# Optimization experiments

Hardware: AMD Instinct MI355X
Metric: run time of the kernel (lower is better)

Reference implementation:

```python
import jax, jax.numpy as jnp
import numpy as np

E = 512        # embed_dim
H = 8          # num_heads
DH = E // H    # head dim
CONCAT = 2 * E # 1024
HID = CONCAT // 2  # 512
OUT = 256      # out_dim
B = 65536


def setup_inputs() -> dict:
    key = jax.random.key(0)
    ks = jax.random.split(key, 12)
    s = lambda fan_in: 1.0 / np.sqrt(fan_in)
    return {
        "visual_emb": jax.random.normal(ks[0], (B, E), jnp.float32),
        "text_emb": jax.random.normal(ks[1], (B, E), jnp.float32),
        # nn.MultiheadAttention params (torch layout: Linear weight is (out,in))
        "in_proj_w": jax.random.uniform(ks[2], (3 * E, E), jnp.float32, -s(E), s(E)),
        "in_proj_b": jnp.zeros((3 * E,), jnp.float32),
        "out_proj_w": jax.random.uniform(ks[3], (E, E), jnp.float32, -s(E), s(E)),
        "out_proj_b": jnp.zeros((E,), jnp.float32),
        # MLP
        "mlp_w1": jax.random.uniform(ks[4], (HID, CONCAT), jnp.float32, -s(CONCAT), s(CONCAT)),
        "mlp_b1": jax.random.uniform(ks[5], (HID,), jnp.float32, -s(CONCAT), s(CONCAT)),
        "mlp_w2": jax.random.uniform(ks[6], (OUT, HID), jnp.float32, -s(HID), s(HID)),
        "mlp_b2": jax.random.uniform(ks[7], (OUT,), jnp.float32, -s(HID), s(HID)),
        # LayerNorm
        "ln_gamma": jnp.ones((OUT,), jnp.float32),
        "ln_beta": jnp.zeros((OUT,), jnp.float32),
    }


def reference(visual_emb, text_emb, in_proj_w, in_proj_b, out_proj_w, out_proj_b,
              mlp_w1, mlp_b1, mlp_w2, mlp_b2, ln_gamma, ln_beta):
    # (B, 2, E) stack of modalities
    x = jnp.stack([visual_emb, text_emb], axis=1)
    # fused QKV projection
    qkv = jnp.einsum("bse,fe->bsf", x, in_proj_w) + in_proj_b  # (B,2,3E)
    q, k, v = jnp.split(qkv, 3, axis=-1)
    # split heads -> (B,H,2,DH)
    split = lambda t: t.reshape(t.shape[0], 2, H, DH).transpose(0, 2, 1, 3)
    q, k, v = split(q), split(k), split(v)
    scores = jnp.einsum("bhqd,bhkd->bhqk", q, k) / jnp.sqrt(jnp.float32(DH))
    attn = jax.nn.softmax(scores, axis=-1)          # (B,H,2,2)
    ctx = jnp.einsum("bhqk,bhkd->bhqd", attn, v)    # (B,H,2,DH)
    ctx = ctx.transpose(0, 2, 1, 3).reshape(-1, 2, E)
    attended = jnp.einsum("bse,fe->bsf", ctx, out_proj_w) + out_proj_b
    weights = attn.mean(axis=1)                     # average over heads (torch default)
    flat = attended.reshape(attended.shape[0], CONCAT)
    h = jax.nn.gelu(flat @ mlp_w1.T + mlp_b1, approximate=False)
    o = h @ mlp_w2.T + mlp_b2                       # (B, OUT)
    mu = o.mean(axis=-1, keepdims=True)
    var = o.var(axis=-1, keepdims=True)
    fused = (o - mu) * jax.lax.rsqrt(var + 1e-5) * ln_gamma + ln_beta
    return fused, weights
```

## Files before the change

### kernel.cpp

```cpp
#include <hip/hip_runtime.h>
#include <hip/hip_bf16.h>
#include <math.h>

#define BATCH   65536L
#define EDIM    512
#define QKVDIM  1536
#define CONCATD 1024
#define HIDD    512
#define OUTD    256

typedef __bf16 bf16_t;
typedef __bf16 bf16x8 __attribute__((ext_vector_type(8)));
typedef __bf16 bf16x4 __attribute__((ext_vector_type(4)));
typedef float  floatx4 __attribute__((ext_vector_type(4)));

static_assert(sizeof(bf16x8) == 16, "bf16x8 must be 16B");

__device__ __forceinline__ void gload16(const void* g, void* l) {
  __builtin_amdgcn_global_load_lds(
      (__attribute__((address_space(1))) void*)(g),
      (__attribute__((address_space(3))) void*)(l), 16, 0, 0);
}

__global__ __launch_bounds__(256) void convert_x_kernel(
    const float* __restrict__ vis, const float* __restrict__ txt,
    bf16_t* __restrict__ dst) {
  long idx = (long)blockIdx.x * 256 + threadIdx.x;
  long t = idx >> 6;
  int  c = (int)(idx & 63) * 8;
  long b = t >> 1;
  const float* src = ((t & 1) ? txt : vis) + b * EDIM + c;
  float4 f0 = *(const float4*)src;
  float4 f1 = *(const float4*)(src + 4);
  bf16x8 o;
  o[0] = (bf16_t)f0.x; o[1] = (bf16_t)f0.y; o[2] = (bf16_t)f0.z; o[3] = (bf16_t)f0.w;
  o[4] = (bf16_t)f1.x; o[5] = (bf16_t)f1.y; o[6] = (bf16_t)f1.z; o[7] = (bf16_t)f1.w;
  *(bf16x8*)(dst + t * EDIM + c) = o;
}

__global__ __launch_bounds__(256) void convert_w_kernel(
    const float* __restrict__ wq, const float* __restrict__ w2,
    bf16_t* __restrict__ dst) {
  long idx = ((long)blockIdx.x * 256 + threadIdx.x) * 8;
  const long n0 = 786432;
  const float* src; long off;
  if (idx < n0) { src = wq; off = idx; }
  else          { src = w2; off = idx - n0; }
  float4 f0 = *(const float4*)(src + off);
  float4 f1 = *(const float4*)(src + off + 4);
  bf16x8 o;
  o[0] = (bf16_t)f0.x; o[1] = (bf16_t)f0.y; o[2] = (bf16_t)f0.z; o[3] = (bf16_t)f0.w;
  o[4] = (bf16_t)f1.x; o[5] = (bf16_t)f1.y; o[6] = (bf16_t)f1.z; o[7] = (bf16_t)f1.w;
  *(bf16x8*)(dst + idx) = o;
}

__global__ __launch_bounds__(256) void wc_kernel(
    const float* __restrict__ w1, const float* __restrict__ wo,
    bf16_t* __restrict__ wc) {
  int n = blockIdx.x;
  int t = threadIdx.x;
  const float* w1v = w1 + (long)n * 1024;
  const float* w1t = w1v + 512;
  float a0 = 0.f, a1 = 0.f, a2 = 0.f, a3 = 0.f;
  for (int f = 0; f < 512; f++) {
    float wv = w1v[f], wt = w1t[f];
    float x0 = wo[f * 512 + t], x1 = wo[f * 512 + t + 256];
    a0 += wv * x0; a1 += wv * x1;
    a2 += wt * x0; a3 += wt * x1;
  }
  bf16_t* out = wc + (long)n * 1024;
  out[t]        = (bf16_t)a0;
  out[t + 256]  = (bf16_t)a1;
  out[t + 512]  = (bf16_t)a2;
  out[t + 768]  = (bf16_t)a3;
}

__global__ __launch_bounds__(256) void bc_kernel(
    const float* __restrict__ w1, const float* __restrict__ bo,
    const float* __restrict__ b1, float* __restrict__ bc) {
  int n = blockIdx.x * 256 + threadIdx.x;
  const float* w1row = w1 + (long)n * 1024;
  float acc = b1[n];
  for (int f = 0; f < 512; f++)
    acc += (w1row[f] + w1row[512 + f]) * bo[f];
  bc[n] = acc;
}

template<int EPI>
__global__ __launch_bounds__(512, 2) void gemm256_kernel(
    const bf16_t* __restrict__ A, const bf16_t* __restrict__ Bt,
    const float* __restrict__ bias, bf16_t* __restrict__ C,
    int M, int N, int K, int ntiles) {
  __shared__ __attribute__((aligned(16))) bf16_t lds[4 * 16384];
  int bid = blockIdx.x;
  {
    const int nwg = gridDim.x;
    if ((nwg & 7) == 0) bid = (bid & 7) * (nwg >> 3) + (bid >> 3);
  }
  const int mt   = bid / ntiles;
  const int nt   = bid % ntiles;
  const int tid  = threadIdx.x;
  const int wave = tid >> 6;
  const int lane = tid & 63;
  const int WM   = wave >> 2;
  const int WN   = wave & 3;

  floatx4 acc[8][4];
  #pragma unroll
  for (int i = 0; i < 8; i++)
    #pragma unroll
    for (int j = 0; j < 4; j++) acc[i][j] = (floatx4){0.f, 0.f, 0.f, 0.f};

  const int srow = wave * 16 + (lane >> 2);
  const int scol = (((lane & 3) ^ ((lane >> 3) & 3)) * 8);
  const bf16_t* Ag0 = A  + (long)(mt * 256 + srow) * K + scol;
  const bf16_t* Ag1 = Ag0 + 128L * K;
  const bf16_t* Bg0 = Bt + (long)(nt * 256 + srow) * K + scol;
  const bf16_t* Bg1 = Bg0 + 128L * K;
  const int woff = wave * 512;

  const int m_l = lane & 15;
  const int kq  = (((lane >> 4) ^ ((m_l >> 1) & 3)) * 8);
  const int Kt  = K >> 5;
  const int Km  = Kt - 1;

#define STAGE(tk, slot) do {                                    \
    const long ko_ = (long)(tk) * 32;                           \
    bf16_t* s_ = lds + (slot) * 16384;                          \
    gload16(Ag0 + ko_, s_ + woff);                              \
    gload16(Ag1 + ko_, s_ + 4096 + woff);                       \
    gload16(Bg0 + ko_, s_ + 8192 + woff);                       \
    gload16(Bg1 + ko_, s_ + 12288 + woff);                      \
  } while (0)

  STAGE(0, 0);
  STAGE(1, 1);
  STAGE(2, 2);

  for (int t = 0; t < Kt; t++) {
    STAGE((t + 3) & Km, (t + 3) & 3);
    asm volatile("s_waitcnt vmcnt(12)" ::: "memory");
    __builtin_amdgcn_s_barrier();
    asm volatile("" ::: "memory");

    const bf16_t* sl = lds + (t & 3) * 16384;
    bf16x8 a[8], b[4];
    #pragma unroll
    for (int i = 0; i < 8; i++)
      a[i] = *(const bf16x8*)&sl[(WM * 128 + i * 16 + m_l) * 32 + kq];
    #pragma unroll
    for (int j = 0; j < 4; j++)
      b[j] = *(const bf16x8*)&sl[8192 + (WN * 64 + j * 16 + m_l) * 32 + kq];
    #pragma unroll
    for (int i = 0; i < 8; i++)
      #pragma unroll
      for (int j = 0; j < 4; j++)
        acc[i][j] = __builtin_amdgcn_mfma_f32_16x16x32_bf16(a[i], b[j], acc[i][j], 0, 0, 0);

    asm volatile("" ::: "memory");
    __builtin_amdgcn_s_barrier();
    asm volatile("" ::: "memory");
  }
#undef STAGE

  const int col_l = lane & 15;
  const int row_q = (lane >> 4) * 4;
  float bj[4];
  #pragma unroll
  for (int j = 0; j < 4; j++)
    bj[j] = bias[nt * 256 + WN * 64 + j * 16 + col_l];
  #pragma unroll
  for (int i = 0; i < 8; i++) {
    #pragma unroll
    for (int r = 0; r < 4; r++) {
      long row = (long)(mt * 256 + WM * 128 + i * 16 + row_q + r);
      bf16_t* crow = C + row * N + nt * 256 + WN * 64 + col_l;
      #pragma unroll
      for (int j = 0; j < 4; j++) {
        float v = acc[i][j][r] + bj[j];
        if (EPI == 1) v = 0.5f * v * (1.0f + erff(v * 0.70710678118654752f));
        crow[j * 16] = (bf16_t)v;
      }
    }
  }
}

__global__ __launch_bounds__(256) void mlp2_ln_kernel(
    const bf16_t* __restrict__ A,
    const bf16_t* __restrict__ Bt,
    const float* __restrict__ bias,
    const float* __restrict__ gamma, const float* __restrict__ beta,
    float* __restrict__ out) {
  __shared__ __attribute__((aligned(16))) char smem[67072];
  bf16_t* sA   = (bf16_t*)smem;
  bf16_t* sB   = (bf16_t*)(smem + 4096);
  float*  Ot   = (float*)smem;
  float*  mu_s = (float*)(smem + 66560);
  float*  rs_s = (float*)(smem + 66816);

  const int tid  = threadIdx.x;
  const int wave = tid >> 6;
  const int lane = tid & 63;

  floatx4 acc[4][4];
  #pragma unroll
  for (int i = 0; i < 4; i++)
    #pragma unroll
    for (int j = 0; j < 4; j++) acc[i][j] = (floatx4){0.f, 0.f, 0.f, 0.f};

  const int srow = wave * 16 + (lane >> 2);
  const int scol = (((lane & 3) ^ ((lane >> 3) & 3)) * 8);
  const bf16_t* Ag = A  + ((long)blockIdx.x * 64 + srow) * 512 + scol;
  const bf16_t* Bg = Bt + (long)srow * 512 + scol;
  bf16_t* sAw = sA + wave * 16 * 32;

  const int m_l = lane & 15;
  const int kq  = (((lane >> 4) ^ ((m_l >> 1) & 3)) * 8);

  for (int k0 = 0; k0 < 512; k0 += 32) {
    __syncthreads();
    gload16(Ag + k0, sAw);
    gload16(Bg + k0,              sB + (0   + wave * 16) * 32);
    gload16(Bg + 64L * 512 + k0,  sB + (64  + wave * 16) * 32);
    gload16(Bg + 128L * 512 + k0, sB + (128 + wave * 16) * 32);
    gload16(Bg + 192L * 512 + k0, sB + (192 + wave * 16) * 32);
    __syncthreads();

    bf16x8 a[4], b[4];
    #pragma unroll
    for (int i = 0; i < 4; i++)
      a[i] = *(const bf16x8*)&sA[(i * 16 + m_l) * 32 + kq];
    #pragma unroll
    for (int j = 0; j < 4; j++)
      b[j] = *(const bf16x8*)&sB[(wave * 64 + j * 16 + m_l) * 32 + kq];
    #pragma unroll
    for (int i = 0; i < 4; i++)
      #pragma unroll
      for (int j = 0; j < 4; j++)
        acc[i][j] = __builtin_amdgcn_mfma_f32_16x16x32_bf16(a[i], b[j], acc[i][j], 0, 0, 0);
  }

  const int col_l = lane & 15;
  const int row_q = (lane >> 4) * 4;
  float bj[4];
  #pragma unroll
  for (int j = 0; j < 4; j++)
    bj[j] = bias[wave * 64 + j * 16 + col_l];
  __syncthreads();
  #pragma unroll
  for (int i = 0; i < 4; i++)
    #pragma unroll
    for (int r = 0; r < 4; r++)
      #pragma unroll
      for (int j = 0; j < 4; j++)
        Ot[(i * 16 + row_q + r) * 260 + wave * 64 + j * 16 + col_l] =
            acc[i][j][r] + bj[j];
  __syncthreads();

  {
    int row = tid >> 2, q = tid & 3;
    const float* p = Ot + row * 260 + q * 64;
    float s = 0.f, s2 = 0.f;
    #pragma unroll
    for (int c = 0; c < 64; c += 4) {
      float4 v = *(const float4*)(p + c);
      s  += v.x + v.y + v.z + v.w;
      s2 += v.x * v.x + v.y * v.y + v.z * v.z + v.w * v.w;
    }
    s  += __shfl_xor(s, 1);  s  += __shfl_xor(s, 2);
    s2 += __shfl_xor(s2, 1); s2 += __shfl_xor(s2, 2);
    if (q == 0) {
      float mu  = s * (1.0f / 256.0f);
      float var = s2 * (1.0f / 256.0f) - mu * mu;
      mu_s[row] = mu;
      rs_s[row] = rsqrtf(var + 1e-5f);
    }
  }
  __syncthreads();

  float4 g  = *(const float4*)(gamma + lane * 4);
  float4 be = *(const float4*)(beta + lane * 4);
  #pragma unroll
  for (int rr = 0; rr < 16; rr++) {
    int row = rr * 4 + wave;
    float mu = mu_s[row], rs = rs_s[row];
    float4 v = *(const float4*)(Ot + row * 260 + lane * 4);
    float4 res;
    res.x = (v.x - mu) * rs * g.x + be.x;
    res.y = (v.y - mu) * rs * g.y + be.y;
    res.z = (v.z - mu) * rs * g.z + be.z;
    res.w = (v.w - mu) * rs * g.w + be.w;
    *(float4*)(out + ((long)blockIdx.x * 64 + row) * 256 + lane * 4) = res;
  }
}

__global__ __launch_bounds__(256) void attn_kernel(
    const bf16_t* __restrict__ qkv, bf16_t* __restrict__ ctx,
    float* __restrict__ wout) {
  const int  lane = threadIdx.x & 63;
  const long b    = (long)blockIdx.x * 4 + (threadIdx.x >> 6);
  const bf16_t* base = qkv + b * 2 * QKVDIM;
  const int off = lane * 8;

  bf16x8 q0 = *(const bf16x8*)(base + off);
  bf16x8 k0 = *(const bf16x8*)(base + EDIM + off);
  bf16x8 v0 = *(const bf16x8*)(base + 2 * EDIM + off);
  bf16x8 q1 = *(const bf16x8*)(base + QKVDIM + off);
  bf16x8 k1 = *(const bf16x8*)(base + QKVDIM + EDIM + off);
  bf16x8 v1 = *(const bf16x8*)(base + QKVDIM + 2 * EDIM + off);

  float s00 = 0.f, s01 = 0.f, s10 = 0.f, s11 = 0.f;
  #pragma unroll
  for (int r = 0; r < 8; r++) {
    float x0 = (float)q0[r], x1 = (float)q1[r];
    float y0 = (float)k0[r], y1 = (float)k1[r];
    s00 += x0 * y0; s01 += x0 * y1; s10 += x1 * y0; s11 += x1 * y1;
  }
  #pragma unroll
  for (int m = 1; m < 8; m <<= 1) {
    s00 += __shfl_xor(s00, m); s01 += __shfl_xor(s01, m);
    s10 += __shfl_xor(s10, m); s11 += __shfl_xor(s11, m);
  }
  const float sc = 0.125f;
  s00 *= sc; s01 *= sc; s10 *= sc; s11 *= sc;
  float m0 = fmaxf(s00, s01), m1 = fmaxf(s10, s11);
  float e00 = __expf(s00 - m0), e01 = __expf(s01 - m0);
  float e10 = __expf(s10 - m1), e11 = __expf(s11 - m1);
  float d0 = e00 + e01, d1 = e10 + e11;
  float a00 = e00 / d0, a01 = e01 / d0, a10 = e10 / d1, a11 = e11 / d1;

  float r00 = a00, r01 = a01, r10 = a10, r11 = a11;
  #pragma unroll
  for (int m = 8; m < 64; m <<= 1) {
    r00 += __shfl_xor(r00, m); r01 += __shfl_xor(r01, m);
    r10 += __shfl_xor(r10, m); r11 += __shfl_xor(r11, m);
  }
  if (lane == 0) {
    float4 wv = make_float4(r00 * 0.125f, r01 * 0.125f, r10 * 0.125f, r11 * 0.125f);
    *(float4*)(wout + b * 4) = wv;
  }

  bf16x8 t0, t1;
  #pragma unroll
  for (int r = 0; r < 8; r++) {
    float f0 = (float)v0[r], f1 = (float)v1[r];
    t0[r] = (bf16_t)(a00 * f0 + a01 * f1);
    t1[r] = (bf16_t)(a10 * f0 + a11 * f1);
  }
  *(bf16x8*)(ctx + (b * 2) * EDIM + off)     = t0;
  *(bf16x8*)(ctx + (b * 2 + 1) * EDIM + off) = t1;
}

extern "C" void kernel_launch(void* const* d_in, const int* in_sizes, int n_in,
                              void* d_out, int out_size, void* d_ws, size_t ws_size,
                              hipStream_t stream) {
  (void)in_sizes; (void)n_in; (void)out_size;
  const float* vis   = (const float*)d_in[0];
  const float* txt   = (const float*)d_in[1];
  const float* w_qkv = (const float*)d_in[2];
  const float* b_qkv = (const float*)d_in[3];
  const float* w_out = (const float*)d_in[4];
  const float* b_out = (const float*)d_in[5];
  const float* w1    = (const float*)d_in[6];
  const float* b1    = (const float*)d_in[7];
  const float* w2    = (const float*)d_in[8];
  const float* b2    = (const float*)d_in[9];
  const float* gamma = (const float*)d_in[10];
  const float* beta  = (const float*)d_in[11];
  float* out_fused   = (float*)d_out;
  float* out_weights = out_fused + BATCH * OUTD;

  char* ws = (char*)d_ws;
  const size_t MB = 1024 * 1024;

  long Bc = BATCH;
  int  nch = 1;
  while (((size_t)(4 * MB) + (size_t)(8192UL * (unsigned long)Bc) > ws_size
          || Bc > 32768) && nch < 64) {
    Bc >>= 1; nch <<= 1;
  }

  bf16_t* wq_b = (bf16_t*)ws;
  bf16_t* w2_b = wq_b + 786432;
  bf16_t* wc_b = wq_b + 917504;
  float*  bc   = (float*)(ws + 3 * MB);
  convert_w_kernel<<<448, 256, 0, stream>>>(w_qkv, w2, wq_b);
  wc_kernel<<<512, 256, 0, stream>>>(w1, w_out, wc_b);
  bc_kernel<<<2, 256, 0, stream>>>(w1, b_out, b1, bc);

  bf16_t* reg1 = (bf16_t*)(ws + 4 * MB);
  bf16_t* reg2 = (bf16_t*)(ws + 4 * MB + (size_t)2048 * Bc);

  const long Tc = 2 * Bc;
  for (int c = 0; c < nch; c++) {
    const float* visc = vis + (long)c * Bc * EDIM;
    const float* txtc = txt + (long)c * Bc * EDIM;
    bf16_t* X   = reg1;
    bf16_t* QKV = reg2;
    bf16_t* CTX = reg1;
    bf16_t* H   = reg2;

    convert_x_kernel<<<(int)(Tc / 4), 256, 0, stream>>>(visc, txtc, X);
    gemm256_kernel<0><<<(int)(Tc / 256) * 6, 512, 0, stream>>>(
        X, wq_b, b_qkv, QKV, (int)Tc, QKVDIM, EDIM, 6);
    attn_kernel<<<(int)(Bc / 4), 256, 0, stream>>>(
        QKV, CTX, out_weights + (long)c * Bc * 4);
    gemm256_kernel<1><<<(int)(Bc / 256) * 2, 512, 0, stream>>>(
        CTX, wc_b, bc, H, (int)Bc, HIDD, CONCATD, 2);
    mlp2_ln_kernel<<<(int)(Bc / 64), 256, 0, stream>>>(
        H, w2_b, b2, gamma, beta, out_fused + (long)c * Bc * OUTD);
  }
}
```

Before: 872.1 us.

## Shrink GEMM tiles to 128x128 with 4 waves and triple-buffered LDS

Replaces the 256x256, 8-wave GEMM with a 128x128, 4-wave version. LDS use drops from a 4-stage to a 3-stage ring with a prefetch distance of 2, and s_setprio is raised around the MFMA block. Smaller tiles and less LDS per block are meant to raise occupancy and spread work more evenly across CUs. In exchange, arithmetic intensity per tile falls, so more global/L2 traffic is spent re-reading A and B.

```diff
diff --git a/kernel.cpp b/kernel.cpp
--- a/kernel.cpp
+++ b/kernel.cpp
@@ -87,11 +87,11 @@
 }
 
 template<int EPI>
-__global__ __launch_bounds__(512, 2) void gemm256_kernel(
+__global__ __launch_bounds__(256, 3) void gemm128_kernel(
     const bf16_t* __restrict__ A, const bf16_t* __restrict__ Bt,
     const float* __restrict__ bias, bf16_t* __restrict__ C,
     int M, int N, int K, int ntiles) {
-  __shared__ __attribute__((aligned(16))) bf16_t lds[4 * 16384];
+  __shared__ __attribute__((aligned(16))) bf16_t lds[3 * 8192];
   int bid = blockIdx.x;
   {
     const int nwg = gridDim.x;
@@ -102,21 +102,21 @@
   const int tid  = threadIdx.x;
   const int wave = tid >> 6;
   const int lane = tid & 63;
-  const int WM   = wave >> 2;
-  const int WN   = wave & 3;
-
-  floatx4 acc[8][4];
-  #pragma unroll
-  for (int i = 0; i < 8; i++)
+  const int wm   = wave >> 1;
+  const int wn   = wave & 1;
+
+  floatx4 acc[4][4];
+  #pragma unroll
+  for (int i = 0; i < 4; i++)
     #pragma unroll
     for (int j = 0; j < 4; j++) acc[i][j] = (floatx4){0.f, 0.f, 0.f, 0.f};
 
   const int srow = wave * 16 + (lane >> 2);
   const int scol = (((lane & 3) ^ ((lane >> 3) & 3)) * 8);
-  const bf16_t* Ag0 = A  + (long)(mt * 256 + srow) * K + scol;
-  const bf16_t* Ag1 = Ag0 + 128L * K;
-  const bf16_t* Bg0 = Bt + (long)(nt * 256 + srow) * K + scol;
-  const bf16_t* Bg1 = Bg0 + 128L * K;
+  const bf16_t* Ag0 = A  + (long)(mt * 128 + srow) * K + scol;
+  const bf16_t* Ag1 = Ag0 + 64L * K;
+  const bf16_t* Bg0 = Bt + (long)(nt * 128 + srow) * K + scol;
+  const bf16_t* Bg1 = Bg0 + 64L * K;
   const int woff = wave * 512;
 
   const int m_l = lane & 15;
@@ -126,40 +126,44 @@
 
 #define STAGE(tk, slot) do {                                    \
     const long ko_ = (long)(tk) * 32;                           \
-    bf16_t* s_ = lds + (slot) * 16384;                          \
+    bf16_t* s_ = lds + (slot) * 8192;                           \
     gload16(Ag0 + ko_, s_ + woff);                              \
-    gload16(Ag1 + ko_, s_ + 4096 + woff);                       \
-    gload16(Bg0 + ko_, s_ + 8192 + woff);                       \
-    gload16(Bg1 + ko_, s_ + 12288 + woff);                      \
+    gload16(Ag1 + ko_, s_ + 2048 + woff);                       \
+    gload16(Bg0 + ko_, s_ + 4096 + woff);                       \
+    gload16(Bg1 + ko_, s_ + 6144 + woff);                       \
   } while (0)
 
   STAGE(0, 0);
   STAGE(1, 1);
-  STAGE(2, 2);
-
+
+  int cur = 0;
   for (int t = 0; t < Kt; t++) {
-    STAGE((t + 3) & Km, (t + 3) & 3);
-    asm volatile("s_waitcnt vmcnt(12)" ::: "memory");
+    int stg = cur + 2; if (stg >= 3) stg -= 3;
+    STAGE((t + 2) & Km, stg);
+    asm volatile("s_waitcnt vmcnt(8)" ::: "memory");
     __builtin_amdgcn_s_barrier();
     asm volatile("" ::: "memory");
 
-    const bf16_t* sl = lds + (t & 3) * 16384;
-    bf16x8 a[8], b[4];
-    #pragma unroll
-    for (int i = 0; i < 8; i++)
-      a[i] = *(const bf16x8*)&sl[(WM * 128 + i * 16 + m_l) * 32 + kq];
+    const bf16_t* sl = lds + cur * 8192;
+    bf16x8 a[4], b[4];
+    #pragma unroll
+    for (int i = 0; i < 4; i++)
+      a[i] = *(const bf16x8*)&sl[(wm * 64 + i * 16 + m_l) * 32 + kq];
     #pragma unroll
     for (int j = 0; j < 4; j++)
-      b[j] = *(const bf16x8*)&sl[8192 + (WN * 64 + j * 16 + m_l) * 32 + kq];
-    #pragma unroll
-    for (int i = 0; i < 8; i++)
+      b[j] = *(const bf16x8*)&sl[4096 + (wn * 64 + j * 16 + m_l) * 32 + kq];
+    __builtin_amdgcn_s_setprio(1);
+    #pragma unroll
+    for (int i = 0; i < 4; i++)
       #pragma unroll
       for (int j = 0; j < 4; j++)
         acc[i][j] = __builtin_amdgcn_mfma_f32_16x16x32_bf16(a[i], b[j], acc[i][j], 0, 0, 0);
+    __builtin_amdgcn_s_setprio(0);
 
     asm volatile("" ::: "memory");
     __builtin_amdgcn_s_barrier();
     asm volatile("" ::: "memory");
+    cur = cur + 1; if (cur >= 3) cur = 0;
   }
 #undef STAGE
 
@@ -168,13 +172,13 @@
   float bj[4];
   #pragma unroll
   for (int j = 0; j < 4; j++)
-    bj[j] = bias[nt * 256 + WN * 64 + j * 16 + col_l];
-  #pragma unroll
-  for (int i = 0; i < 8; i++) {
+    bj[j] = bias[nt * 128 + wn * 64 + j * 16 + col_l];
+  #pragma unroll
+  for (int i = 0; i < 4; i++) {
     #pragma unroll
     for (int r = 0; r < 4; r++) {
-      long row = (long)(mt * 256 + WM * 128 + i * 16 + row_q + r);
-      bf16_t* crow = C + row * N + nt * 256 + WN * 64 + col_l;
+      long row = (long)(mt * 128 + wm * 64 + i * 16 + row_q + r);
+      bf16_t* crow = C + row * N + nt * 128 + wn * 64 + col_l;
       #pragma unroll
       for (int j = 0; j < 4; j++) {
         float v = acc[i][j][r] + bj[j];
@@ -401,12 +405,12 @@
     bf16_t* H   = reg2;
 
     convert_x_kernel<<<(int)(Tc / 4), 256, 0, stream>>>(visc, txtc, X);
-    gemm256_kernel<0><<<(int)(Tc / 256) * 6, 512, 0, stream>>>(
-        X, wq_b, b_qkv, QKV, (int)Tc, QKVDIM, EDIM, 6);
+    gemm128_kernel<0><<<(int)(Tc / 128) * 12, 256, 0, stream>>>(
+        X, wq_b, b_qkv, QKV, (int)Tc, QKVDIM, EDIM, 12);
     attn_kernel<<<(int)(Bc / 4), 256, 0, stream>>>(
         QKV, CTX, out_weights + (long)c * Bc * 4);
-    gemm256_kernel<1><<<(int)(Bc / 256) * 2, 512, 0, stream>>>(
-        CTX, wc_b, bc, H, (int)Bc, HIDD, CONCATD, 2);
+    gemm128_kernel<1><<<(int)(Bc / 128) * 4, 256, 0, stream>>>(
+        CTX, wc_b, bc, H, (int)Bc, HIDD, CONCATD, 4);
     mlp2_ln_kernel<<<(int)(Bc / 64), 256, 0, stream>>>(
         H, w2_b, b2, gamma, beta, out_fused + (long)c * Bc * OUTD);
   }
```

New measurement: 877.8 us. No clear change (+0.7%).
